# Kernel optimization log

Measured on AMD Instinct MI355X. Metric: run time of the kernel, lower is better.

Reference implementation:

```python
import jax, jax.numpy as jnp
import numpy as np

G = 8            # group_order
KS = 3           # kernel size
C1, O1 = 1, 16   # gconv1 channels
C2, O2 = 16, 32  # gconv2 channels
HW = 28
NUM_CLASSES = 10


def _bilinear_sample(img, px, py):
    # img: (O, I, K, K); px, py: (K, K) pixel coords; zero padding outside
    # (matches torch grid_sample bilinear, align_corners=False, padding_mode='zeros')
    K = img.shape[-1]
    x0 = jnp.floor(px); y0 = jnp.floor(py)
    wx = px - x0; wy = py - y0
    x0i = x0.astype(jnp.int32); y0i = y0.astype(jnp.int32)

    def gather(yi, xi):
        valid = (yi >= 0) & (yi < K) & (xi >= 0) & (xi < K)
        yc = jnp.clip(yi, 0, K - 1)
        xc = jnp.clip(xi, 0, K - 1)
        return img[:, :, yc, xc] * valid.astype(img.dtype)  # (O,I,K,K)

    return (gather(y0i, x0i) * (1 - wx) * (1 - wy)
            + gather(y0i, x0i + 1) * wx * (1 - wy)
            + gather(y0i + 1, x0i) * (1 - wx) * wy
            + gather(y0i + 1, x0i + 1) * wx * wy)


def _rotated_kernels(base, group_order):
    # Replicates F.affine_grid + F.grid_sample (align_corners=False) for each rotation k.
    K = base.shape[-1]
    coords = (2.0 * jnp.arange(K, dtype=base.dtype) + 1.0) / K - 1.0  # normalized centers
    xs, ys = jnp.meshgrid(coords, coords, indexing='xy')  # x along width, y along height

    def rot_k(k):
        theta = 2.0 * np.pi * k / group_order
        c, s = jnp.cos(theta), jnp.sin(theta)
        gx = c * xs - s * ys   # theta row [cos, -sin, 0]
        gy = s * xs + c * ys   # theta row [sin,  cos, 0]
        px = ((gx + 1.0) * K - 1.0) / 2.0  # unnormalize, align_corners=False
        py = ((gy + 1.0) * K - 1.0) / 2.0
        return _bilinear_sample(base, px, py)

    return jax.vmap(rot_k)(jnp.arange(group_order, dtype=base.dtype))  # (G,O,I,K,K)


def _conv2d(x, w, pad):
    return jax.lax.conv_general_dilated(
        x, w, window_strides=(1, 1), padding=[(pad, pad), (pad, pad)],
        dimension_numbers=('NCHW', 'OIHW', 'NCHW'))


def setup_inputs() -> dict:
    key = jax.random.key(0)
    k1, k2, k3, k4, k5 = jax.random.split(key, 5)
    x = jax.random.normal(k1, (512, C1, HW, HW), dtype=jnp.float32)
    base_weight = jax.random.normal(k2, (O1, C1, KS, KS), dtype=jnp.float32)
    w2 = jax.random.normal(k3, (O2, C2, G, KS, KS), dtype=jnp.float32) * 0.05
    fc_w = jax.random.normal(k4, (NUM_CLASSES, O2 * HW * HW), dtype=jnp.float32) * 0.01
    fc_b = jax.random.normal(k5, (NUM_CLASSES,), dtype=jnp.float32) * 0.01
    return {"x": x, "base_weight": base_weight, "w2": w2, "fc_w": fc_w, "fc_b": fc_b}


def reference(x, base_weight, w2, fc_w, fc_b):
    B = x.shape[0]
    # --- GroupConv2D: steerable rotated kernels, concat along out-channels (k-major) ---
    rk = _rotated_kernels(base_weight, G)           # (G, O1, C1, K, K)
    w1 = rk.reshape(G * O1, C1, KS, KS)
    h = _conv2d(x, w1, 1)                           # (B, G*O1, 28, 28)
    h = jax.nn.relu(h)                              # GroupReLU == plain ReLU

    # --- GroupToGroupConv: circulant structure fused into one conv ---
    # torch: out channel = g*O2 + o (cat dim=1), in channel = c*G + h_idx (view layout)
    g = jnp.arange(G)[:, None]
    hh = jnp.arange(G)[None, :]
    idx = (g - hh) % G                               # (G, G)
    Wc = w2[:, :, idx]                               # (O2, C2, G_g, G_h, K, K)
    Wbig = jnp.transpose(Wc, (2, 0, 1, 3, 4, 5)).reshape(G * O2, C2 * G, KS, KS)
    h2 = _conv2d(h, Wbig, 1)                         # (B, G*O2, 28, 28)
    h2 = jax.nn.relu(h2)

    # --- GroupPooling (mean over the *inner* factor of 8, as in the torch view) ---
    p = h2.reshape(B, (G * O2) // G, G, HW, HW).mean(axis=2)  # (B, 32, 28, 28)

    # --- fc ---
    flat = p.reshape(B, -1)
    return flat @ fc_w.T + fc_b
```

## Files before the change

### kernel.cpp

```cpp
#include <hip/hip_runtime.h>
#include <hip/hip_bf16.h>
#include <cstdint>

#define AS1 __attribute__((address_space(1)))
#define AS3 __attribute__((address_space(3)))

typedef __bf16 bf16x8 __attribute__((ext_vector_type(8)));
typedef float  f32x16 __attribute__((ext_vector_type(16)));

__device__ __forceinline__ void gld_lds16(const void* g, void* l) {
    __builtin_amdgcn_global_load_lds((const AS1 void*)g, (AS3 void*)l, 16, 0, 0);
}

__global__ __launch_bounds__(256) void k_conv1(const float* __restrict__ x,
                                               const float* __restrict__ base,
                                               const float* __restrict__ w2,
                                               __hip_bfloat16* __restrict__ hl,
                                               __hip_bfloat16* __restrict__ A) {
    int tid = threadIdx.x;

    if (blockIdx.x < 1152) {
        int i = blockIdx.x * 256 + tid;
        int r = i / 1152, k = i - r * 1152;
        int g = r >> 5, o2 = r & 31;
        int kk = k >> 7, cch = k & 127;
        int ky = kk / 3, kx = kk - ky * 3;
        int c2 = cch >> 3, hh = cch & 7;
        int gi = (g - hh) & 7;
        A[i] = __float2bfloat16(w2[((o2 * 16 + c2) * 8 + gi) * 9 + ky * 3 + kx]);
    }

    __shared__ float w1s[1152];
    if (tid < 128) {
        int g = tid >> 4, o = tid & 15;
        float th = 6.28318530717958647692f * (float)g / 8.0f;
        float c = cosf(th), s = sinf(th);
        for (int i = 0; i < 3; ++i) {
            float ys = (2.0f * i + 1.0f) / 3.0f - 1.0f;
            for (int j = 0; j < 3; ++j) {
                float xs = (2.0f * j + 1.0f) / 3.0f - 1.0f;
                float gx = c * xs - s * ys;
                float gy = s * xs + c * ys;
                float px = ((gx + 1.0f) * 3.0f - 1.0f) * 0.5f;
                float py = ((gy + 1.0f) * 3.0f - 1.0f) * 0.5f;
                float x0 = floorf(px), y0 = floorf(py);
                float wx = px - x0, wy = py - y0;
                int x0i = (int)x0, y0i = (int)y0;
                auto gat = [&](int yi, int xi) -> float {
                    bool v = (yi >= 0) && (yi < 3) && (xi >= 0) && (xi < 3);
                    int yc = min(max(yi, 0), 2), xc = min(max(xi, 0), 2);
                    return v ? base[o * 9 + yc * 3 + xc] : 0.0f;
                };
                w1s[tid * 9 + i * 3 + j] =
                      gat(y0i, x0i)         * (1.0f - wx) * (1.0f - wy)
                    + gat(y0i, x0i + 1)     * wx          * (1.0f - wy)
                    + gat(y0i + 1, x0i)     * (1.0f - wx) * wy
                    + gat(y0i + 1, x0i + 1) * wx          * wy;
            }
        }
    }
    __syncthreads();

    const int c0 = (tid & 15) * 8;
    float wreg[8][9];
#pragma unroll
    for (int cc = 0; cc < 8; ++cc)
#pragma unroll
        for (int k = 0; k < 9; ++k) wreg[cc][k] = w1s[(c0 + cc) * 9 + k];

    const int ps = tid >> 4;
    const int pbase = blockIdx.x * 64;

#pragma unroll
    for (int j = 0; j < 4; ++j) {
        int pi = pbase + j * 16 + ps;
        int xx = pi % 30; int t = pi / 30; int yy = t % 30; int b = t / 30;
        float acc[8] = {0.f,0.f,0.f,0.f,0.f,0.f,0.f,0.f};
        if (xx >= 1 && xx <= 28 && yy >= 1 && yy <= 28) {
            const float* xb = x + b * 784;
            int y = yy - 1, xc = xx - 1;
#pragma unroll
            for (int dy = -1; dy <= 1; ++dy) {
                int sy = y + dy;
#pragma unroll
                for (int dx = -1; dx <= 1; ++dx) {
                    int sx = xc + dx;
                    float xv = (sy >= 0 && sy < 28 && sx >= 0 && sx < 28) ? xb[sy * 28 + sx] : 0.0f;
                    int k = (dy + 1) * 3 + (dx + 1);
#pragma unroll
                    for (int cc = 0; cc < 8; ++cc) acc[cc] += xv * wreg[cc][k];
                }
            }
        }
        union { __hip_bfloat16 h[8]; float4 f4; } u;
#pragma unroll
        for (int cc = 0; cc < 8; ++cc) u.h[cc] = __float2bfloat16(fmaxf(acc[cc], 0.0f));
        *(float4*)(hl + (size_t)pi * 128 + c0) = u.f4;
    }
}

__global__ __launch_bounds__(256) void k_conv2(const __hip_bfloat16* __restrict__ A,
                                               const __hip_bfloat16* __restrict__ hl,
                                               __hip_bfloat16* __restrict__ p) {
    __shared__ __align__(16) char smem[32768];

    const int tid  = threadIdx.x;
    const int lane = tid & 63;
    const int w    = tid >> 6;
    const int wr   = w >> 1, wc = w & 1;
    const int hi   = lane >> 5;

    const int bid  = blockIdx.x;
    const int xcd  = bid & 7;
    const int slot = bid >> 3;
    const int nt   = xcd + 8 * (slot >> 1);
    const int mt   = slot & 1;
    const int n0 = nt << 7;
    const int r0 = mt << 7;

    uint32_t aG[4], bG[4], ldsOff[4];
#pragma unroll
    for (int q = 0; q < 4; ++q) {
        int ch = w * 4 + q;
        int rl = ch * 8 + (lane >> 3);
        int ca = (lane & 7) ^ (rl & 7) ^ (ch & 3);
        aG[q] = (uint32_t)((r0 + rl) * 2304 + ca * 16);
        int n  = n0 + rl;
        int b  = n / 784; int rr = n - b * 784;
        int y  = rr / 28; int xx = rr - y * 28;
        bG[q]  = (uint32_t)(((b * 30 + y) * 30 + xx) * 256 + ca * 16);
        ldsOff[q] = (uint32_t)(ch * 1024);
    }

    uint32_t aro[2], bro[2]; int asw[2], bsw[2];
#pragma unroll
    for (int t = 0; t < 2; ++t) {
        int rl = 64 * wr + 32 * t + (lane & 31);
        aro[t] = (uint32_t)(rl * 128); asw[t] = (rl & 7) ^ ((rl >> 3) & 3);
        int nl = 64 * wc + 32 * t + (lane & 31);
        bro[t] = (uint32_t)(16384 + nl * 128); bsw[t] = (nl & 7) ^ ((nl >> 3) & 3);
    }

    f32x16 acc[2][2];
#pragma unroll
    for (int i = 0; i < 2; ++i)
#pragma unroll
        for (int j = 0; j < 2; ++j) acc[i][j] = (f32x16)(0.0f);

    const char* Ab = (const char*)A;
    const char* Hb = (const char*)hl;

    for (int s = 0; s < 18; ++s) {
        int kk = s >> 1, half = s & 1;
        int ky = kk / 3, kx = kk - ky * 3;
        int aoff = kk * 256 + half * 128;
        int boff = (ky * 30 + kx) * 256 + half * 128;

        __syncthreads();
#pragma unroll
        for (int q = 0; q < 4; ++q) {
            gld_lds16(Ab + aG[q] + aoff, smem + ldsOff[q]);
            gld_lds16(Hb + bG[q] + boff, smem + 16384 + ldsOff[q]);
        }
        __syncthreads();

#pragma unroll
        for (int kstep = 0; kstep < 4; ++kstep) {
            int cb = kstep * 2 + hi;
            bf16x8 af[2], bf[2];
#pragma unroll
            for (int t = 0; t < 2; ++t) {
                af[t] = *(const bf16x8*)(smem + aro[t] + ((cb ^ asw[t]) * 16));
                bf[t] = *(const bf16x8*)(smem + bro[t] + ((cb ^ bsw[t]) * 16));
            }
#pragma unroll
            for (int i = 0; i < 2; ++i)
#pragma unroll
                for (int j = 0; j < 2; ++j)
                    acc[i][j] = __builtin_amdgcn_mfma_f32_32x32x16_bf16(af[i], bf[j], acc[i][j], 0, 0, 0);
        }
    }

#pragma unroll
    for (int ti = 0; ti < 2; ++ti) {
        int gbase = (r0 + 64 * wr + 32 * ti) >> 3;
#pragma unroll
        for (int tj = 0; tj < 2; ++tj) {
            f32x16 v = acc[ti][tj];
#pragma unroll
            for (int q = 0; q < 4; ++q) {
                float s = fmaxf(v[4*q], 0.0f) + fmaxf(v[4*q+1], 0.0f)
                        + fmaxf(v[4*q+2], 0.0f) + fmaxf(v[4*q+3], 0.0f);
                s += __shfl_xor(s, 32, 64);
                if (hi == 0) {
                    int a = gbase + q;
                    int n = n0 + 64 * wc + 32 * tj + (lane & 31);
                    int b = n / 784; int rr = n - b * 784;
                    p[(b * 32 + a) * 784 + rr] = __float2bfloat16(s * 0.125f);
                }
            }
        }
    }
}

__global__ __launch_bounds__(256) void k_fc(const __hip_bfloat16* __restrict__ p,
                                            const float* __restrict__ fw,
                                            const float* __restrict__ fb,
                                            float* __restrict__ out) {
    __shared__ float4 wl[3920];
    const int bb = blockIdx.x >> 4;
    const int ks = blockIdx.x & 15;
    const int tid = threadIdx.x;
    const float4* w4 = (const float4*)fw;
    for (int i = tid; i < 3920; i += 256) {
        int c = i / 392, j = i - c * 392;
        wl[i] = w4[c * 6272 + ks * 392 + j];
    }
    __syncthreads();

    const int kl = tid & 15, bi = tid >> 4;
    const int b = bb * 16 + bi;
    const bf16x8* pb = (const bf16x8*)(p + (size_t)b * 25088 + ks * 1568);
    float acc[10] = {};
    for (int t = kl; t < 196; t += 16) {
        union { bf16x8 v; __hip_bfloat16 h[8]; } u;
        u.v = pb[t];
        float vf[8];
#pragma unroll
        for (int e = 0; e < 8; ++e) vf[e] = __bfloat162float(u.h[e]);
#pragma unroll
        for (int c = 0; c < 10; ++c) {
            float4 u0 = wl[c * 392 + 2 * t];
            float4 u1 = wl[c * 392 + 2 * t + 1];
            acc[c] += vf[0] * u0.x + vf[1] * u0.y + vf[2] * u0.z + vf[3] * u0.w
                    + vf[4] * u1.x + vf[5] * u1.y + vf[6] * u1.z + vf[7] * u1.w;
        }
    }
#pragma unroll
    for (int c = 0; c < 10; ++c) {
        float s = acc[c];
        s += __shfl_down(s, 8, 16);
        s += __shfl_down(s, 4, 16);
        s += __shfl_down(s, 2, 16);
        s += __shfl_down(s, 1, 16);
        if (kl == 0) {
            if (ks == 0) s += fb[c];
            atomicAdd(&out[b * 10 + c], s);
        }
    }
}

extern "C" void kernel_launch(void* const* d_in, const int* in_sizes, int n_in,
                              void* d_out, int out_size, void* d_ws, size_t ws_size,
                              hipStream_t stream) {
    const float* x  = (const float*)d_in[0];
    const float* bw = (const float*)d_in[1];
    const float* w2 = (const float*)d_in[2];
    const float* fw = (const float*)d_in[3];
    const float* fb = (const float*)d_in[4];
    float* out = (float*)d_out;
    char* ws = (char*)d_ws;

    __hip_bfloat16* Amat = (__hip_bfloat16*)(ws + 4608);
    __hip_bfloat16* hl   = (__hip_bfloat16*)(ws + 594432);
    __hip_bfloat16* p    = (__hip_bfloat16*)(ws + 118563328);

    hipMemsetAsync(d_out, 0, (size_t)out_size * sizeof(float), stream);
    k_conv1<<<7200, 256, 0, stream>>>(x, bw, w2, hl, Amat);
    k_conv2<<<6272, 256, 0, stream>>>(Amat, hl, p);
    k_fc   <<<512,  256, 0, stream>>>(p, fw, fb, out);
}
```

Before: 392.4 us.

## Enlarge conv2 GEMM tile to full 256 output rows per block

Each conv2 block now computes all 256 output channels for its 128-pixel tile rather than splitting M across two blocks. The activation tile loaded into LDS is reused across twice as many rows, which halves redundant activation loads and halves the grid size. In exchange, LDS use per block rises to 48KB and each wave holds 8 accumulator tiles, which costs registers and may reduce occupancy. The XCD-aware block swizzle is also dropped.

Result: slower. 513.6 us (+30.9%).

```diff
diff --git a/kernel.cpp b/kernel.cpp
--- a/kernel.cpp
+++ b/kernel.cpp
@@ -102,7 +102,7 @@
 __global__ __launch_bounds__(256) void k_conv2(const __hip_bfloat16* __restrict__ A,
                                                const __hip_bfloat16* __restrict__ hl,
                                                __hip_bfloat16* __restrict__ p) {
-    __shared__ __align__(16) char smem[32768];
+    __shared__ __align__(16) char smem[49152];
 
     const int tid  = threadIdx.x;
     const int lane = tid & 63;
@@ -110,40 +110,43 @@
     const int wr   = w >> 1, wc = w & 1;
     const int hi   = lane >> 5;
 
-    const int bid  = blockIdx.x;
-    const int xcd  = bid & 7;
-    const int slot = bid >> 3;
-    const int nt   = xcd + 8 * (slot >> 1);
-    const int mt   = slot & 1;
+    const int nt = blockIdx.x;
     const int n0 = nt << 7;
-    const int r0 = mt << 7;
-
-    uint32_t aG[4], bG[4], ldsOff[4];
+
+    uint32_t aG[8], bG[4];
+#pragma unroll
+    for (int q = 0; q < 8; ++q) {
+        int ch = w * 8 + q;
+        int rl = ch * 8 + (lane >> 3);
+        int ca = (lane & 7) ^ (lane >> 3) ^ (ch & 3);
+        aG[q] = (uint32_t)(rl * 2304 + ca * 16);
+    }
 #pragma unroll
     for (int q = 0; q < 4; ++q) {
         int ch = w * 4 + q;
         int rl = ch * 8 + (lane >> 3);
-        int ca = (lane & 7) ^ (rl & 7) ^ (ch & 3);
-        aG[q] = (uint32_t)((r0 + rl) * 2304 + ca * 16);
+        int ca = (lane & 7) ^ (lane >> 3) ^ (ch & 3);
         int n  = n0 + rl;
         int b  = n / 784; int rr = n - b * 784;
         int y  = rr / 28; int xx = rr - y * 28;
         bG[q]  = (uint32_t)(((b * 30 + y) * 30 + xx) * 256 + ca * 16);
-        ldsOff[q] = (uint32_t)(ch * 1024);
-    }
-
-    uint32_t aro[2], bro[2]; int asw[2], bsw[2];
-#pragma unroll
-    for (int t = 0; t < 2; ++t) {
-        int rl = 64 * wr + 32 * t + (lane & 31);
-        aro[t] = (uint32_t)(rl * 128); asw[t] = (rl & 7) ^ ((rl >> 3) & 3);
-        int nl = 64 * wc + 32 * t + (lane & 31);
-        bro[t] = (uint32_t)(16384 + nl * 128); bsw[t] = (nl & 7) ^ ((nl >> 3) & 3);
-    }
-
-    f32x16 acc[2][2];
-#pragma unroll
-    for (int i = 0; i < 2; ++i)
+    }
+
+    uint32_t aro[4], bro[2]; int asw[4], bsw[2];
+#pragma unroll
+    for (int i = 0; i < 4; ++i) {
+        int rl = 128 * wr + 32 * i + (lane & 31);
+        aro[i] = (uint32_t)(rl * 128); asw[i] = (rl & 7) ^ ((rl >> 3) & 3);
+    }
+#pragma unroll
+    for (int j = 0; j < 2; ++j) {
+        int nl = 64 * wc + 32 * j + (lane & 31);
+        bro[j] = (uint32_t)(32768 + nl * 128); bsw[j] = (nl & 7) ^ ((nl >> 3) & 3);
+    }
+
+    f32x16 acc[4][2];
+#pragma unroll
+    for (int i = 0; i < 4; ++i)
 #pragma unroll
         for (int j = 0; j < 2; ++j) acc[i][j] = (f32x16)(0.0f);
 
@@ -158,23 +161,25 @@
 
         __syncthreads();
 #pragma unroll
-        for (int q = 0; q < 4; ++q) {
-            gld_lds16(Ab + aG[q] + aoff, smem + ldsOff[q]);
-            gld_lds16(Hb + bG[q] + boff, smem + 16384 + ldsOff[q]);
-        }
+        for (int q = 0; q < 8; ++q)
+            gld_lds16(Ab + aG[q] + aoff, smem + (w * 8 + q) * 1024);
+#pragma unroll
+        for (int q = 0; q < 4; ++q)
+            gld_lds16(Hb + bG[q] + boff, smem + 32768 + (w * 4 + q) * 1024);
         __syncthreads();
 
 #pragma unroll
         for (int kstep = 0; kstep < 4; ++kstep) {
             int cb = kstep * 2 + hi;
-            bf16x8 af[2], bf[2];
-#pragma unroll
-            for (int t = 0; t < 2; ++t) {
-                af[t] = *(const bf16x8*)(smem + aro[t] + ((cb ^ asw[t]) * 16));
-                bf[t] = *(const bf16x8*)(smem + bro[t] + ((cb ^ bsw[t]) * 16));
-            }
-#pragma unroll
-            for (int i = 0; i < 2; ++i)
+            bf16x8 af[4], bf[2];
+#pragma unroll
+            for (int i = 0; i < 4; ++i)
+                af[i] = *(const bf16x8*)(smem + aro[i] + ((cb ^ asw[i]) * 16));
+#pragma unroll
+            for (int j = 0; j < 2; ++j)
+                bf[j] = *(const bf16x8*)(smem + bro[j] + ((cb ^ bsw[j]) * 16));
+#pragma unroll
+            for (int i = 0; i < 4; ++i)
 #pragma unroll
                 for (int j = 0; j < 2; ++j)
                     acc[i][j] = __builtin_amdgcn_mfma_f32_32x32x16_bf16(af[i], bf[j], acc[i][j], 0, 0, 0);
@@ -182,19 +187,18 @@
     }
 
 #pragma unroll
-    for (int ti = 0; ti < 2; ++ti) {
-        int gbase = (r0 + 64 * wr + 32 * ti) >> 3;
-#pragma unroll
-        for (int tj = 0; tj < 2; ++tj) {
-            f32x16 v = acc[ti][tj];
+    for (int i = 0; i < 4; ++i) {
+#pragma unroll
+        for (int j = 0; j < 2; ++j) {
+            f32x16 v = acc[i][j];
 #pragma unroll
             for (int q = 0; q < 4; ++q) {
                 float s = fmaxf(v[4*q], 0.0f) + fmaxf(v[4*q+1], 0.0f)
                         + fmaxf(v[4*q+2], 0.0f) + fmaxf(v[4*q+3], 0.0f);
                 s += __shfl_xor(s, 32, 64);
                 if (hi == 0) {
-                    int a = gbase + q;
-                    int n = n0 + 64 * wc + 32 * tj + (lane & 31);
+                    int a = 16 * wr + 4 * i + q;
+                    int n = n0 + 64 * wc + 32 * j + (lane & 31);
                     int b = n / 784; int rr = n - b * 784;
                     p[(b * 32 + a) * 784 + rr] = __float2bfloat16(s * 0.125f);
                 }
@@ -267,6 +271,6 @@
 
     hipMemsetAsync(d_out, 0, (size_t)out_size * sizeof(float), stream);
     k_conv1<<<7200, 256, 0, stream>>>(x, bw, w2, hl, Amat);
-    k_conv2<<<6272, 256, 0, stream>>>(Amat, hl, p);
+    k_conv2<<<3136, 256, 0, stream>>>(Amat, hl, p);
     k_fc   <<<512,  256, 0, stream>>>(p, fw, fb, out);
 }
```
